# Kernel optimization log

Hardware: AMD Instinct MI355X
Metric: run time of the kernel (lower is better)

Reference implementation:

```python
import jax, jax.numpy as jnp
import numpy as np

B = 4
N1_PER = 16384  # fine points per scene
N2_PER = 4096   # coarse points per scene
IN_PLANES = 512
OUT_PLANES = 256
K = 3
CHUNK = 2048
BN_EPS = 1e-5


def _bn(x, g, b, m, v):
    # eval-mode BatchNorm1d: affine normalize with running stats
    return (x - m) * (g / jnp.sqrt(v + BN_EPS)) + b


def _interpolate_one(p1b, p2b, f2b):
    # p1b: [n1,3] queries, p2b: [n2,3] support, f2b: [n2,C]
    # k=3 inverse-distance weighted interpolation (pointops.interpolation)
    pq = p1b.reshape(-1, CHUNK, 3)  # chunk queries to avoid full [n1,n2] matrix

    def step(carry, q):  # q: [CHUNK,3]
        d2 = jnp.sum((q[:, None, :] - p2b[None, :, :]) ** 2, axis=-1)  # [CHUNK,n2]
        neg_d2, idx = jax.lax.top_k(-d2, K)                            # [CHUNK,K]
        dist = jnp.sqrt(jnp.maximum(-neg_d2, 1e-12))
        w = 1.0 / (dist + 1e-8)
        w = w / jnp.sum(w, axis=-1, keepdims=True)
        feat = f2b[idx]  # [CHUNK,K,C] gather
        return carry, jnp.einsum('qk,qkc->qc', w, feat)

    _, out = jax.lax.scan(step, None, pq)
    return out.reshape(-1, f2b.shape[-1])  # [n1,C]


def _forward(p1, x1, p2, x2, W1, b1, g1, be1, m1, v1, W2, b2, g2, be2, m2, v2):
    # branch 1: Linear-BN-ReLU on fine features
    h1 = jax.nn.relu(_bn(x1 @ W1.T + b1, g1, be1, m1, v1))  # [N1, out]
    # branch 2: Linear-BN-ReLU on coarse features, then kNN interpolation up
    h2 = jax.nn.relu(_bn(x2 @ W2.T + b2, g2, be2, m2, v2))  # [N2, out]
    # equal-sized scenes -> reshape + vmap over batch (offsets are [n,2n,...])
    p1b = p1.reshape(B, N1_PER, 3)
    p2b = p2.reshape(B, N2_PER, 3)
    h2b = h2.reshape(B, N2_PER, -1)
    up = jax.vmap(_interpolate_one)(p1b, p2b, h2b).reshape(-1, h2.shape[-1])
    return h1 + up


def setup_inputs() -> dict:
    key = jax.random.key(0)
    ks = jax.random.split(key, 16)
    p1 = jax.random.normal(ks[0], (B * N1_PER, 3), dtype=jnp.float32)
    x1 = jax.random.normal(ks[1], (B * N1_PER, OUT_PLANES), dtype=jnp.float32)
    p2 = jax.random.normal(ks[2], (B * N2_PER, 3), dtype=jnp.float32)
    x2 = jax.random.normal(ks[3], (B * N2_PER, IN_PLANES), dtype=jnp.float32)
    o1 = (jnp.arange(1, B + 1) * N1_PER).astype(jnp.int64)
    o2 = (jnp.arange(1, B + 1) * N2_PER).astype(jnp.int64)
    s1 = 1.0 / np.sqrt(OUT_PLANES)
    s2 = 1.0 / np.sqrt(IN_PLANES)
    W1 = jax.random.uniform(ks[4], (OUT_PLANES, OUT_PLANES), minval=-s1, maxval=s1)
    b1 = jax.random.uniform(ks[5], (OUT_PLANES,), minval=-s1, maxval=s1)
    W2 = jax.random.uniform(ks[6], (OUT_PLANES, IN_PLANES), minval=-s2, maxval=s2)
    b2 = jax.random.uniform(ks[7], (OUT_PLANES,), minval=-s2, maxval=s2)
    g1 = jnp.ones((OUT_PLANES,)); be1 = jnp.zeros((OUT_PLANES,))
    m1 = 0.1 * jax.random.normal(ks[8], (OUT_PLANES,))
    v1 = jax.random.uniform(ks[9], (OUT_PLANES,), minval=0.5, maxval=1.5)
    g2 = jnp.ones((OUT_PLANES,)); be2 = jnp.zeros((OUT_PLANES,))
    m2 = 0.1 * jax.random.normal(ks[10], (OUT_PLANES,))
    v2 = jax.random.uniform(ks[11], (OUT_PLANES,), minval=0.5, maxval=1.5)
    return dict(p1=p1, x1=x1, p2=p2, x2=x2, W1=W1, b1=b1, g1=g1, be1=be1,
                m1=m1, v1=v1, W2=W2, b2=b2, g2=g2, be2=be2, m2=m2, v2=v2,
                o1=o1, o2=o2)


def reference(p1, x1, p2, x2, W1, b1, g1, be1, m1, v1, W2, b2, g2, be2, m2, v2, o1, o2):
    return _forward(p1, x1, p2, x2, W1, b1, g1, be1, m1, v1, W2, b2, g2, be2, m2, v2)
```

## Files before the change

kernel.cpp:

```cpp
#include <hip/hip_runtime.h>

#define BM 128
#define BNT 128
#define BK 32
#define LDK 40

typedef __bf16 bf16x8 __attribute__((ext_vector_type(8)));
typedef float  f32x4  __attribute__((ext_vector_type(4)));
typedef float  f32x2  __attribute__((ext_vector_type(2)));

static __device__ __forceinline__ unsigned short f2bf(float f) {
  union { float f; unsigned int i; } c; c.f = f;
  unsigned int u = c.i;
  u += 0x7FFFu + ((u >> 16) & 1u);
  return (unsigned short)(u >> 16);
}

#define SEG0 16777216u
#define SEG1 25165824u
#define SEG2 25231360u
#define SEG3 25362432u

__global__ __launch_bounds__(256) void cvt4_k(const float* __restrict__ s0,
                                              const float* __restrict__ s1,
                                              const float* __restrict__ s2,
                                              const float* __restrict__ s3,
                                              unsigned short* __restrict__ dst) {
  const unsigned int e = (blockIdx.x * 256u + threadIdx.x) * 8u;
  const float* sp; unsigned int off;
  if (e < SEG0)      { sp = s0; off = e; }
  else if (e < SEG1) { sp = s1; off = e - SEG0; }
  else if (e < SEG2) { sp = s2; off = e - SEG1; }
  else               { sp = s3; off = e - SEG2; }
  const float4* p = (const float4*)(sp + off);
  const float4 a = p[0], b = p[1];
  uint4 o;
  o.x = ((unsigned int)f2bf(a.y) << 16) | f2bf(a.x);
  o.y = ((unsigned int)f2bf(a.w) << 16) | f2bf(a.z);
  o.z = ((unsigned int)f2bf(b.y) << 16) | f2bf(b.x);
  o.w = ((unsigned int)f2bf(b.w) << 16) | f2bf(b.z);
  *(uint4*)(dst + e) = o;
}

template<bool FUSE>
__global__ __launch_bounds__(256) void gemm_bn_relu_k(
    const unsigned short* __restrict__ A,
    const unsigned short* __restrict__ Wm,
    const float* __restrict__ bias,
    const float* __restrict__ gam,
    const float* __restrict__ bet,
    const float* __restrict__ rmean,
    const float* __restrict__ rvar,
    const int K,
    float* __restrict__ outp,
    const float* __restrict__ h2f,
    const float* __restrict__ wgt,
    const int* __restrict__ idxg)
{
  __shared__ unsigned short As[BM][LDK];
  __shared__ unsigned short Bs[BNT][LDK];
  __shared__ float SC[BNT];
  __shared__ float SH[BNT];
  __shared__ float Wt[BM * 3];
  __shared__ int   Id[BM * 3];

  const int tid = threadIdx.x;
  const int bm = blockIdx.x, bn = blockIdx.y;

  if (tid < BNT) {
    const int ch = bn * BNT + tid;
    const float sc = gam[ch] / sqrtf(rvar[ch] + 1e-5f);
    SC[tid] = sc;
    SH[tid] = (bias[ch] - rmean[ch]) * sc + bet[ch];
  }
  if (FUSE) {
    for (int i = tid; i < BM * 3; i += 256) {
      Wt[i] = wgt[bm * (BM * 3) + i];
      Id[i] = idxg[bm * (BM * 3) + i];
    }
  }

  const int wave = tid >> 6, lane = tid & 63;
  const int wr = (wave >> 1) * 64, wc = (wave & 1) * 64;
  const int lr = lane & 15;
  const int kq = (lane >> 4) * 8;

  const int r0 = tid >> 2, co = (tid & 3) * 8;
  const int r1 = 64 + r0;
  const unsigned short* Ar0 = A + (size_t)(bm * BM + r0) * K + co;
  const unsigned short* Ar1 = A + (size_t)(bm * BM + r1) * K + co;
  const unsigned short* Br0 = Wm + (size_t)(bn * BNT + r0) * K + co;
  const unsigned short* Br1 = Wm + (size_t)(bn * BNT + r1) * K + co;

  f32x4 acc[4][4];
  const f32x4 zero = {0.f, 0.f, 0.f, 0.f};
#pragma unroll
  for (int i = 0; i < 4; ++i)
#pragma unroll
    for (int j = 0; j < 4; ++j) acc[i][j] = zero;

  uint4 va0 = *(const uint4*)(Ar0);
  uint4 va1 = *(const uint4*)(Ar1);
  uint4 vb0 = *(const uint4*)(Br0);
  uint4 vb1 = *(const uint4*)(Br1);

  for (int k0 = 0; k0 < K; k0 += BK) {
    __syncthreads();
    *(uint4*)&As[r0][co] = va0;
    *(uint4*)&As[r1][co] = va1;
    *(uint4*)&Bs[r0][co] = vb0;
    *(uint4*)&Bs[r1][co] = vb1;
    __syncthreads();
    if (k0 + BK < K) {
      va0 = *(const uint4*)(Ar0 + k0 + BK);
      va1 = *(const uint4*)(Ar1 + k0 + BK);
      vb0 = *(const uint4*)(Br0 + k0 + BK);
      vb1 = *(const uint4*)(Br1 + k0 + BK);
    }
    bf16x8 af[4], bv[4];
#pragma unroll
    for (int mi = 0; mi < 4; ++mi)
      af[mi] = *(const bf16x8*)&As[wr + mi * 16 + lr][kq];
#pragma unroll
    for (int ni = 0; ni < 4; ++ni)
      bv[ni] = *(const bf16x8*)&Bs[wc + ni * 16 + lr][kq];
#pragma unroll
    for (int mi = 0; mi < 4; ++mi)
#pragma unroll
      for (int ni = 0; ni < 4; ++ni)
        acc[mi][ni] = __builtin_amdgcn_mfma_f32_16x16x32_bf16(af[mi], bv[ni], acc[mi][ni], 0, 0, 0);
  }

#pragma unroll
  for (int mi = 0; mi < 4; ++mi) {
#pragma unroll
    for (int r = 0; r < 4; ++r) {
      const int rloc = wr + mi * 16 + (lane >> 4) * 4 + r;
      const size_t grow = (size_t)(bm * BM + rloc);
      float w0 = 0.f, w1 = 0.f, w2 = 0.f;
      const float *g0 = nullptr, *g1 = nullptr, *g2 = nullptr;
      if (FUSE) {
        w0 = Wt[rloc * 3 + 0]; w1 = Wt[rloc * 3 + 1]; w2 = Wt[rloc * 3 + 2];
        g0 = h2f + (size_t)Id[rloc * 3 + 0] * 256;
        g1 = h2f + (size_t)Id[rloc * 3 + 1] * 256;
        g2 = h2f + (size_t)Id[rloc * 3 + 2] * 256;
      }
#pragma unroll
      for (int ni = 0; ni < 4; ++ni) {
        const int cloc = wc + ni * 16 + lr;
        const int gcol = bn * BNT + cloc;
        float v = acc[mi][ni][r] * SC[cloc] + SH[cloc];
        v = fmaxf(v, 0.f);
        if (FUSE) v += w0 * g0[gcol] + w1 * g1[gcol] + w2 * g2[gcol];
        outp[grow * 256 + gcol] = v;
      }
    }
  }
}

__global__ __launch_bounds__(256) void prep_pairs(const float* __restrict__ p2,
                                                  float* __restrict__ pp) {
  const int m = blockIdx.x * 256 + threadIdx.x;
  const float* s = p2 + m * 6;
  float* d = pp + m * 8;
  d[0] = s[0]; d[1] = s[3];
  d[2] = s[1]; d[3] = s[4];
  d[4] = s[2]; d[5] = s[5];
  d[6] = 0.f;  d[7] = 0.f;
}

__global__ __launch_bounds__(256) void knn_partial(const float* __restrict__ p1,
                                                   const float* __restrict__ ppair,
                                                   float* __restrict__ s_part,
                                                   int* __restrict__ i_part) {
#pragma clang fp contract(off)
  const int tid = threadIdx.x;
  const int qb = blockIdx.x, sp = blockIdx.y;
  const int scene = qb >> 6;
  const int pbase = scene * 4096 + sp * 512;
  const int qi = qb * 256 + tid;

  const float qx = p1[qi * 3 + 0];
  const float qy = p1[qi * 3 + 1];
  const float qz = p1[qi * 3 + 2];
  const f32x2 qxx = {qx, qx}, qyy = {qy, qy}, qzz = {qz, qz};

  float s0 = 1e30f, s1 = 1e30f, s2 = 1e30f;
  int i0 = pbase, i1 = pbase, i2 = pbase;

  const f32x2* pp = (const f32x2*)(ppair + (size_t)(pbase >> 1) * 8);
#pragma unroll 4
  for (int m = 0; m < 256; ++m) {
    const f32x2 X = pp[m * 4 + 0];
    const f32x2 Y = pp[m * 4 + 1];
    const f32x2 Z = pp[m * 4 + 2];
    const f32x2 dx = qxx - X;
    const f32x2 dy = qyy - Y;
    const f32x2 dz = qzz - Z;
    const f32x2 sv = (dx * dx + dy * dy) + dz * dz;
    const int jg = pbase + 2 * m;
    const float sa = sv.x, sb = sv.y;
    if (sa < s2) {
      if (sa < s1) {
        s2 = s1; i2 = i1;
        if (sa < s0) { s1 = s0; i1 = i0; s0 = sa; i0 = jg; }
        else         { s1 = sa; i1 = jg; }
      } else { s2 = sa; i2 = jg; }
    }
    if (sb < s2) {
      if (sb < s1) {
        s2 = s1; i2 = i1;
        if (sb < s0) { s1 = s0; i1 = i0; s0 = sb; i0 = jg + 1; }
        else         { s1 = sb; i1 = jg + 1; }
      } else { s2 = sb; i2 = jg + 1; }
    }
  }
  const int ob = (qi * 8 + sp) * 3;
  s_part[ob + 0] = s0; s_part[ob + 1] = s1; s_part[ob + 2] = s2;
  i_part[ob + 0] = i0; i_part[ob + 1] = i1; i_part[ob + 2] = i2;
}

__global__ __launch_bounds__(256) void knn_merge(const float* __restrict__ s_part,
                                                 const int* __restrict__ i_part,
                                                 float* __restrict__ wgt,
                                                 int* __restrict__ idxg) {
  const int qi = blockIdx.x * 256 + threadIdx.x;

  float s0 = 1e30f, s1 = 1e30f, s2 = 1e30f;
  int i0 = 0, i1 = 0, i2 = 0;
  const int base = qi * 24;
#pragma unroll
  for (int t = 0; t < 24; ++t) {
    const float s = s_part[base + t];
    const int id = i_part[base + t];
    if (s < s2) {
      if (s < s1) {
        s2 = s1; i2 = i1;
        if (s < s0) { s1 = s0; i1 = i0; s0 = s; i0 = id; }
        else        { s1 = s;  i1 = id; }
      } else { s2 = s; i2 = id; }
    }
  }
  const float d0 = sqrtf(fmaxf(s0, 1e-12f));
  const float d1 = sqrtf(fmaxf(s1, 1e-12f));
  const float d2 = sqrtf(fmaxf(s2, 1e-12f));
  float w0 = 1.f / (d0 + 1e-8f);
  float w1 = 1.f / (d1 + 1e-8f);
  float w2 = 1.f / (d2 + 1e-8f);
  const float inv = 1.f / (w0 + w1 + w2);
  wgt[qi * 3 + 0] = w0 * inv; wgt[qi * 3 + 1] = w1 * inv; wgt[qi * 3 + 2] = w2 * inv;
  idxg[qi * 3 + 0] = i0; idxg[qi * 3 + 1] = i1; idxg[qi * 3 + 2] = i2;
}

extern "C" void kernel_launch(void* const* d_in, const int* in_sizes, int n_in,
                              void* d_out, int out_size, void* d_ws, size_t ws_size,
                              hipStream_t stream) {
  const float* p1 = (const float*)d_in[0];
  const float* x1 = (const float*)d_in[1];
  const float* p2 = (const float*)d_in[2];
  const float* x2 = (const float*)d_in[3];
  const float* W1 = (const float*)d_in[4];
  const float* b1 = (const float*)d_in[5];
  const float* g1 = (const float*)d_in[6];
  const float* be1 = (const float*)d_in[7];
  const float* m1 = (const float*)d_in[8];
  const float* v1 = (const float*)d_in[9];
  const float* W2 = (const float*)d_in[10];
  const float* b2 = (const float*)d_in[11];
  const float* g2 = (const float*)d_in[12];
  const float* be2 = (const float*)d_in[13];
  const float* m2 = (const float*)d_in[14];
  const float* v2 = (const float*)d_in[15];

  char* ws = (char*)d_ws;
  unsigned short* bfb = (unsigned short*)ws;
  unsigned short* x1b = bfb;
  unsigned short* x2b = bfb + SEG0;
  unsigned short* W1b = bfb + SEG1;
  unsigned short* W2b = bfb + SEG2;
  float* s_part = (float*)(ws + 33554432);
  int*   i_part = (int*)(ws + 39845888);
  float* h2f    = (float*)(ws + 50724864);
  float* ppair  = (float*)(ws + 67502080);
  float* wgt    = (float*)(ws + 67764224);
  int*   idxg   = (int*)(ws + 68550656);

  float* outp = (float*)d_out;

  cvt4_k<<<12384, 256, 0, stream>>>(x1, x2, W1, W2, bfb);

  gemm_bn_relu_k<false><<<dim3(128, 2), 256, 0, stream>>>(
      x2b, W2b, b2, g2, be2, m2, v2, 512, h2f, nullptr, nullptr, nullptr);

  prep_pairs<<<32, 256, 0, stream>>>(p2, ppair);

  knn_partial<<<dim3(256, 8), 256, 0, stream>>>(p1, ppair, s_part, i_part);

  knn_merge<<<256, 256, 0, stream>>>(s_part, i_part, wgt, idxg);

  gemm_bn_relu_k<true><<<dim3(512, 2), 256, 0, stream>>>(
      x1b, W1b, b1, g1, be1, m1, v1, 256, outp, h2f, wgt, idxg);
}
```

Measured before the change: 338.3 us.

## Fuse activation bf16 conversion into GEMM loads and halve kNN split count

```diff
diff --git a/kernel.cpp b/kernel.cpp
--- a/kernel.cpp
+++ b/kernel.cpp
@@ -16,35 +16,32 @@
   return (unsigned short)(u >> 16);
 }
 
-#define SEG0 16777216u
-#define SEG1 25165824u
-#define SEG2 25231360u
-#define SEG3 25362432u
-
-__global__ __launch_bounds__(256) void cvt4_k(const float* __restrict__ s0,
-                                              const float* __restrict__ s1,
-                                              const float* __restrict__ s2,
-                                              const float* __restrict__ s3,
-                                              unsigned short* __restrict__ dst) {
-  const unsigned int e = (blockIdx.x * 256u + threadIdx.x) * 8u;
-  const float* sp; unsigned int off;
-  if (e < SEG0)      { sp = s0; off = e; }
-  else if (e < SEG1) { sp = s1; off = e - SEG0; }
-  else if (e < SEG2) { sp = s2; off = e - SEG1; }
-  else               { sp = s3; off = e - SEG2; }
-  const float4* p = (const float4*)(sp + off);
-  const float4 a = p[0], b = p[1];
+static __device__ __forceinline__ uint4 pk8(const float4 a, const float4 b) {
   uint4 o;
   o.x = ((unsigned int)f2bf(a.y) << 16) | f2bf(a.x);
   o.y = ((unsigned int)f2bf(a.w) << 16) | f2bf(a.z);
   o.z = ((unsigned int)f2bf(b.y) << 16) | f2bf(b.x);
   o.w = ((unsigned int)f2bf(b.w) << 16) | f2bf(b.z);
-  *(uint4*)(dst + e) = o;
+  return o;
+}
+
+#define WSEG0 65536u
+#define WSEG1 196608u
+
+__global__ __launch_bounds__(256) void cvt_w(const float* __restrict__ s0,
+                                             const float* __restrict__ s1,
+                                             unsigned short* __restrict__ dst) {
+  const unsigned int e = (blockIdx.x * 256u + threadIdx.x) * 8u;
+  const float* sp; unsigned int off;
+  if (e < WSEG0) { sp = s0; off = e; }
+  else           { sp = s1; off = e - WSEG0; }
+  const float4* p = (const float4*)(sp + off);
+  *(uint4*)(dst + e) = pk8(p[0], p[1]);
 }
 
 template<bool FUSE>
 __global__ __launch_bounds__(256) void gemm_bn_relu_k(
-    const unsigned short* __restrict__ A,
+    const float* __restrict__ A,
     const unsigned short* __restrict__ Wm,
     const float* __restrict__ bias,
     const float* __restrict__ gam,
@@ -87,8 +84,8 @@
 
   const int r0 = tid >> 2, co = (tid & 3) * 8;
   const int r1 = 64 + r0;
-  const unsigned short* Ar0 = A + (size_t)(bm * BM + r0) * K + co;
-  const unsigned short* Ar1 = A + (size_t)(bm * BM + r1) * K + co;
+  const float* Ar0 = A + (size_t)(bm * BM + r0) * K + co;
+  const float* Ar1 = A + (size_t)(bm * BM + r1) * K + co;
   const unsigned short* Br0 = Wm + (size_t)(bn * BNT + r0) * K + co;
   const unsigned short* Br1 = Wm + (size_t)(bn * BNT + r1) * K + co;
 
@@ -99,21 +96,25 @@
 #pragma unroll
     for (int j = 0; j < 4; ++j) acc[i][j] = zero;
 
-  uint4 va0 = *(const uint4*)(Ar0);
-  uint4 va1 = *(const uint4*)(Ar1);
+  float4 fa00 = *(const float4*)(Ar0);
+  float4 fa01 = *(const float4*)(Ar0 + 4);
+  float4 fa10 = *(const float4*)(Ar1);
+  float4 fa11 = *(const float4*)(Ar1 + 4);
   uint4 vb0 = *(const uint4*)(Br0);
   uint4 vb1 = *(const uint4*)(Br1);
 
   for (int k0 = 0; k0 < K; k0 += BK) {
     __syncthreads();
-    *(uint4*)&As[r0][co] = va0;
-    *(uint4*)&As[r1][co] = va1;
+    *(uint4*)&As[r0][co] = pk8(fa00, fa01);
+    *(uint4*)&As[r1][co] = pk8(fa10, fa11);
     *(uint4*)&Bs[r0][co] = vb0;
     *(uint4*)&Bs[r1][co] = vb1;
     __syncthreads();
     if (k0 + BK < K) {
-      va0 = *(const uint4*)(Ar0 + k0 + BK);
-      va1 = *(const uint4*)(Ar1 + k0 + BK);
+      fa00 = *(const float4*)(Ar0 + k0 + BK);
+      fa01 = *(const float4*)(Ar0 + k0 + BK + 4);
+      fa10 = *(const float4*)(Ar1 + k0 + BK);
+      fa11 = *(const float4*)(Ar1 + k0 + BK + 4);
       vb0 = *(const uint4*)(Br0 + k0 + BK);
       vb1 = *(const uint4*)(Br1 + k0 + BK);
     }
@@ -177,7 +178,7 @@
   const int tid = threadIdx.x;
   const int qb = blockIdx.x, sp = blockIdx.y;
   const int scene = qb >> 6;
-  const int pbase = scene * 4096 + sp * 512;
+  const int pbase = scene * 4096 + sp * 1024;
   const int qi = qb * 256 + tid;
 
   const float qx = p1[qi * 3 + 0];
@@ -190,7 +191,7 @@
 
   const f32x2* pp = (const f32x2*)(ppair + (size_t)(pbase >> 1) * 8);
 #pragma unroll 4
-  for (int m = 0; m < 256; ++m) {
+  for (int m = 0; m < 512; ++m) {
     const f32x2 X = pp[m * 4 + 0];
     const f32x2 Y = pp[m * 4 + 1];
     const f32x2 Z = pp[m * 4 + 2];
@@ -215,7 +216,7 @@
       } else { s2 = sb; i2 = jg + 1; }
     }
   }
-  const int ob = (qi * 8 + sp) * 3;
+  const int ob = (qi * 4 + sp) * 3;
   s_part[ob + 0] = s0; s_part[ob + 1] = s1; s_part[ob + 2] = s2;
   i_part[ob + 0] = i0; i_part[ob + 1] = i1; i_part[ob + 2] = i2;
 }
@@ -228,9 +229,9 @@
 
   float s0 = 1e30f, s1 = 1e30f, s2 = 1e30f;
   int i0 = 0, i1 = 0, i2 = 0;
-  const int base = qi * 24;
-#pragma unroll
-  for (int t = 0; t < 24; ++t) {
+  const int base = qi * 12;
+#pragma unroll
+  for (int t = 0; t < 12; ++t) {
     const float s = s_part[base + t];
     const int id = i_part[base + t];
     if (s < s2) {
@@ -273,31 +274,28 @@
   const float* v2 = (const float*)d_in[15];
 
   char* ws = (char*)d_ws;
-  unsigned short* bfb = (unsigned short*)ws;
-  unsigned short* x1b = bfb;
-  unsigned short* x2b = bfb + SEG0;
-  unsigned short* W1b = bfb + SEG1;
-  unsigned short* W2b = bfb + SEG2;
-  float* s_part = (float*)(ws + 33554432);
-  int*   i_part = (int*)(ws + 39845888);
-  float* h2f    = (float*)(ws + 50724864);
-  float* ppair  = (float*)(ws + 67502080);
-  float* wgt    = (float*)(ws + 67764224);
-  int*   idxg   = (int*)(ws + 68550656);
+  unsigned short* W1b = (unsigned short*)ws;
+  unsigned short* W2b = (unsigned short*)(ws + 131072);
+  float* s_part = (float*)(ws + 1048576);
+  int*   i_part = (int*)(ws + 4194304);
+  float* h2f    = (float*)(ws + 8388608);
+  float* ppair  = (float*)(ws + 25165824);
+  float* wgt    = (float*)(ws + 25427968);
+  int*   idxg   = (int*)(ws + 26214400);
 
   float* outp = (float*)d_out;
 
-  cvt4_k<<<12384, 256, 0, stream>>>(x1, x2, W1, W2, bfb);
+  cvt_w<<<96, 256, 0, stream>>>(W1, W2, W1b);
 
   gemm_bn_relu_k<false><<<dim3(128, 2), 256, 0, stream>>>(
-      x2b, W2b, b2, g2, be2, m2, v2, 512, h2f, nullptr, nullptr, nullptr);
+      x2, W2b, b2, g2, be2, m2, v2, 512, h2f, nullptr, nullptr, nullptr);
 
   prep_pairs<<<32, 256, 0, stream>>>(p2, ppair);
 
-  knn_partial<<<dim3(256, 8), 256, 0, stream>>>(p1, ppair, s_part, i_part);
+  knn_partial<<<dim3(256, 4), 256, 0, stream>>>(p1, ppair, s_part, i_part);
 
   knn_merge<<<256, 256, 0, stream>>>(s_part, i_part, wgt, idxg);
 
   gemm_bn_relu_k<true><<<dim3(512, 2), 256, 0, stream>>>(
-      x1b, W1b, b1, g1, be1, m1, v1, 256, outp, h2f, wgt, idxg);
-}
+      x1, W1b, b1, g1, be1, m1, v1, 256, outp, h2f, wgt, idxg);
+}
```

Measured after the change: 347.4 us. +2.7%, slower.
